# Kernel tuning notes

Measured on AMD Instinct MI355X. Metric: run time of the kernel, lower is better.

The kernel has to match this reference:

```python
import jax, jax.numpy as jnp
import numpy as np

NUM_USERS = 25000
NUM_ITEMS = 25000
N_NODES = NUM_USERS + NUM_ITEMS
N_EDGES = 800000
EMBED_K = 64
N_LAYERS = 3
LRELU_ALPHA = 0.2  # tf.nn.leaky_relu default
EPS = 1e-12        # tf.nn.l2_normalize default epsilon


def setup_inputs() -> dict:
    key = jax.random.key(0)
    ks = jax.random.split(key, 12)
    return {
        "adj_rows": jax.random.randint(ks[0], (N_EDGES,), 0, N_NODES, dtype=jnp.int32),
        "adj_cols": jax.random.randint(ks[1], (N_EDGES,), 0, N_NODES, dtype=jnp.int32),
        "adj_vals": jax.random.uniform(ks[2], (N_EDGES,), dtype=jnp.float32),
        "Gu0": jax.random.normal(ks[3], (NUM_USERS, EMBED_K), dtype=jnp.float32) * 0.1,
        "Gi0": jax.random.normal(ks[4], (NUM_ITEMS, EMBED_K), dtype=jnp.float32) * 0.1,
        "W_gc": jax.random.normal(ks[5], (N_LAYERS, EMBED_K, EMBED_K), dtype=jnp.float32) * 0.1,
        "b_gc": jax.random.normal(ks[6], (N_LAYERS, EMBED_K), dtype=jnp.float32) * 0.1,
        "W_bi": jax.random.normal(ks[7], (N_LAYERS, EMBED_K, EMBED_K), dtype=jnp.float32) * 0.1,
        "b_bi": jax.random.normal(ks[8], (N_LAYERS, EMBED_K), dtype=jnp.float32) * 0.1,
        "user": jax.random.randint(ks[9], (4096,), 0, NUM_USERS, dtype=jnp.int32),
        "item": jax.random.randint(ks[10], (4096,), 0, NUM_ITEMS, dtype=jnp.int32),
    }


def _propagate(adj_rows, adj_cols, adj_vals, Gu0, Gi0, W_gc, b_gc, W_bi, b_bi):
    # ego: [N, d] concatenation of user + item 0th-layer embeddings
    ego = jnp.concatenate([Gu0, Gi0], axis=0)
    all_embeddings = [ego]
    for k in range(W_gc.shape[0]):
        # sparse A_hat @ ego via COO gather + segment_sum (replaces folded sparse_dense_matmul)
        side = jax.ops.segment_sum(adj_vals[:, None] * ego[adj_cols], adj_rows,
                                   num_segments=N_NODES)
        sum_emb = jax.nn.leaky_relu(side @ W_gc[k] + b_gc[k][None, :], LRELU_ALPHA)
        bi_emb = jax.nn.leaky_relu((ego * side) @ W_bi[k] + b_bi[k][None, :], LRELU_ALPHA)
        ego = sum_emb + bi_emb  # message_dropout = 0 -> identity
        norm = ego * jax.lax.rsqrt(
            jnp.maximum(jnp.sum(ego * ego, axis=1, keepdims=True), EPS))
        all_embeddings.append(norm)
        # NOTE: next layer consumes the UN-normalized ego, as in the original
    all_embeddings = jnp.concatenate(all_embeddings, axis=1)  # [N, d*(L+1)]
    gu = all_embeddings[:NUM_USERS]
    gi = all_embeddings[NUM_USERS:]
    return gu, gi


def reference(adj_rows, adj_cols, adj_vals, Gu0, Gi0, W_gc, b_gc, W_bi, b_bi, user, item):
    gu, gi = _propagate(adj_rows, adj_cols, adj_vals, Gu0, Gi0, W_gc, b_gc, W_bi, b_bi)
    # call(): embedding lookup + dot product per (user, item) pair
    gamma_u = gu[user]
    gamma_i = gi[item]
    xui = jnp.sum(gamma_u * gamma_i, axis=1)
    return xui, gu, gi
```

## Files before the change

### kernel.cpp

```cpp
#include <hip/hip_runtime.h>

#define NUM_USERS 25000
#define NUM_ITEMS 25000
#define N_NODES   50000
#define N_EDGES   800000
#define K         64
#define N_QUERY   4096
#define LRELU     0.2f

#define NBUCKET   196
#define A1_CHUNK  8192
#define A2_CHUNK  4096
#define BMAX      4608

typedef unsigned short ushort_t;
typedef unsigned long long u64_t;

__device__ __forceinline__ size_t node_out_offset(int n) {
    return (size_t)N_QUERY + (size_t)n * 256;
}

__device__ __forceinline__ ushort_t f2bf(float x) {
    unsigned u = __float_as_uint(x);
    return (ushort_t)((u + 0x7FFFu + ((u >> 16) & 1u)) >> 16);
}
__device__ __forceinline__ float bf2f(ushort_t v) {
    return __uint_as_float(((unsigned)v) << 16);
}

__global__ __launch_bounds__(256) void init_ego_kernel(
    const float* __restrict__ Gu0, const float* __restrict__ Gi0,
    float* __restrict__ ego, ushort_t* __restrict__ egb, float* __restrict__ out)
{
    int tid = blockIdx.x * 256 + threadIdx.x;
    if (tid >= N_NODES * K) return;
    int n = tid >> 6;
    int d = tid & 63;
    float v = (n < NUM_USERS) ? Gu0[tid] : Gi0[tid - NUM_USERS * K];
    ego[tid] = v;
    egb[tid] = f2bf(v);
    out[node_out_offset(n) + d] = v;
}

__global__ __launch_bounds__(256) void wtrans_kernel(
    const float* __restrict__ W_gc, const float* __restrict__ W_bi,
    float* __restrict__ WT)
{
    int tid = blockIdx.x * 256 + threadIdx.x;
    if (tid >= 3 * 2 * 64 * 64) return;
    int k   = tid >> 13;
    int m   = (tid >> 12) & 1;
    int idx = tid & 4095;
    int o   = idx >> 6;
    int j   = idx & 63;
    const float* src = m ? W_bi : W_gc;
    WT[tid] = src[k * 4096 + j * 64 + o];
}

__global__ __launch_bounds__(256) void bhist_kernel(
    const int* __restrict__ rows, int* __restrict__ bucket_count)
{
    __shared__ int h[NBUCKET];
    int t = threadIdx.x;
    if (t < NBUCKET) h[t] = 0;
    __syncthreads();
    int base = blockIdx.x * A1_CHUNK;
    for (int i = t; i < A1_CHUNK; i += 256) {
        int e = base + i;
        if (e < N_EDGES) atomicAdd(&h[rows[e] >> 8], 1);
    }
    __syncthreads();
    if (t < NBUCKET) atomicAdd(&bucket_count[t], h[t]);
}

__global__ __launch_bounds__(256) void bscan_kernel(
    const int* __restrict__ bucket_count,
    int* __restrict__ gbase, int* __restrict__ cursor)
{
    __shared__ int sh[256];
    int t = threadIdx.x;
    sh[t] = (t < NBUCKET) ? bucket_count[t] : 0;
    __syncthreads();
    for (int off = 1; off < 256; off <<= 1) {
        int v = (t >= off) ? sh[t - off] : 0;
        __syncthreads();
        sh[t] += v;
        __syncthreads();
    }
    int excl = (t == 0) ? 0 : sh[t - 1];
    if (t < NBUCKET) { gbase[t] = excl; cursor[t] = excl; }
    if (t == NBUCKET) gbase[NBUCKET] = N_EDGES;
}

__global__ __launch_bounds__(256) void bscatter_kernel(
    const int* __restrict__ rows, const int* __restrict__ cols,
    const float* __restrict__ vals, int* __restrict__ cursor,
    u64_t* __restrict__ csr64)
{
    __shared__ u64_t recs[A2_CHUNK];
    __shared__ int hist[NBUCKET], lbase[NBUCKET], lcur[NBUCKET];
    int t = threadIdx.x;
    if (t < NBUCKET) { hist[t] = 0; lcur[t] = 0; }
    __syncthreads();
    int base = blockIdx.x * A2_CHUNK;
    for (int i = t; i < A2_CHUNK; i += 256) {
        int e = base + i;
        if (e < N_EDGES) {
            int r = rows[e];
            u64_t rec = ((u64_t)(unsigned)__float_as_uint(vals[e]) << 32)
                      | ((u64_t)(unsigned)cols[e] << 16)
                      | (unsigned)r;
            recs[i] = rec;
            atomicAdd(&hist[r >> 8], 1);
        }
    }
    __syncthreads();
    if (t < NBUCKET) lbase[t] = atomicAdd(&cursor[t], hist[t]);
    __syncthreads();
    for (int i = t; i < A2_CHUNK; i += 256) {
        int e = base + i;
        if (e < N_EDGES) {
            u64_t rec = recs[i];
            int b = (int)((rec >> 8) & 0xFF);
            int dst = lbase[b] + atomicAdd(&lcur[b], 1);
            csr64[dst] = rec;
        }
    }
}

__global__ __launch_bounds__(256) void bsort_kernel(
    const int* __restrict__ gbase, u64_t* __restrict__ csr64,
    int* __restrict__ offs)
{
    __shared__ u64_t recs[BMAX];
    __shared__ int hist[256], lscan[256], lcur[256];
    int b = blockIdx.x, t = threadIdx.x;
    int g0 = gbase[b];
    int nb = gbase[b + 1] - g0;
    if (nb > BMAX) nb = BMAX;
    hist[t] = 0; lcur[t] = 0;
    __syncthreads();
    for (int i = t; i < nb; i += 256) {
        u64_t rec = csr64[g0 + i];
        recs[i] = rec;
        atomicAdd(&hist[(int)(rec & 0xFF)], 1);
    }
    __syncthreads();
    int v0 = hist[t];
    lscan[t] = v0;
    __syncthreads();
    for (int off = 1; off < 256; off <<= 1) {
        int v = (t >= off) ? lscan[t - off] : 0;
        __syncthreads();
        lscan[t] += v;
        __syncthreads();
    }
    int excl = lscan[t] - v0;
    int row = (b << 8) + t;
    if (row < N_NODES) offs[row] = g0 + excl;
    if (b == 0 && t == 0) offs[N_NODES] = N_EDGES;
    __syncthreads();
    lscan[t] = excl;
    __syncthreads();
    for (int i = t; i < nb; i += 256) {
        u64_t rec = recs[i];
        int rl = (int)(rec & 0xFF);
        int pos = lscan[rl] + atomicAdd(&lcur[rl], 1);
        u64_t outrec = (rec >> 32 << 32) | ((rec >> 16) & 0xFFFFu);
        csr64[g0 + pos] = outrec;
    }
}

__global__ __launch_bounds__(512, 8) void gather_kernel(
    const int* __restrict__ offs, const long long* __restrict__ csr_cv,
    const ushort_t* __restrict__ egb, float* __restrict__ side)
{
    int t = threadIdx.x;
    int wave = t >> 6;
    int lane = t & 63;
    int node = blockIdx.x * 8 + wave;

    int beg = offs[node];
    int end = offs[node + 1];
    float acc = 0.f;
    int j = beg;

    for (; j + 12 <= end; j += 12) {
        long long cvp[12];
        #pragma unroll
        for (int u = 0; u < 12; ++u) cvp[u] = __builtin_nontemporal_load(csr_cv + j + u);
        float gg[12];
        #pragma unroll
        for (int u = 0; u < 12; ++u)
            gg[u] = bf2f(egb[((size_t)(unsigned int)(cvp[u] & 0xffffffffLL) << 6) + lane]);
        #pragma unroll
        for (int u = 0; u < 12; ++u)
            acc = fmaf(__uint_as_float((unsigned int)((u64_t)cvp[u] >> 32)), gg[u], acc);
    }
    for (; j + 4 <= end; j += 4) {
        long long cvp[4];
        #pragma unroll
        for (int u = 0; u < 4; ++u) cvp[u] = __builtin_nontemporal_load(csr_cv + j + u);
        float gg[4];
        #pragma unroll
        for (int u = 0; u < 4; ++u)
            gg[u] = bf2f(egb[((size_t)(unsigned int)(cvp[u] & 0xffffffffLL) << 6) + lane]);
        #pragma unroll
        for (int u = 0; u < 4; ++u)
            acc = fmaf(__uint_as_float((unsigned int)((u64_t)cvp[u] >> 32)), gg[u], acc);
    }
    for (; j < end; ++j) {
        long long cvp = __builtin_nontemporal_load(csr_cv + j);
        acc = fmaf(__uint_as_float((unsigned int)((u64_t)cvp >> 32)),
                   bf2f(egb[((size_t)(unsigned int)(cvp & 0xffffffffLL) << 6) + lane]), acc);
    }

    side[((size_t)node << 6) + lane] = acc;
}

__global__ __launch_bounds__(256, 2) void transform_kernel(
    const float* __restrict__ side, float* __restrict__ ego,
    ushort_t* __restrict__ egb,
    const float* __restrict__ WgT, const float* __restrict__ WbT,
    const float* __restrict__ bgc, const float* __restrict__ bbi,
    float* __restrict__ out, int layer_k)
{
    __shared__ float s_s [64 * 64];
    __shared__ float s_es[64 * 64];
    __shared__ float s_wg[64 * 64];
    __shared__ float s_wb[64 * 64];

    int t = threadIdx.x;
    int base = blockIdx.x * 64;

    for (int idx = t; idx < 64 * 16; idx += 256) {
        int r = idx >> 4;
        int q = idx & 15;
        int qs = q ^ ((r >> 2) & 7);
        float4 sv = make_float4(0.f, 0.f, 0.f, 0.f);
        float4 ev = make_float4(0.f, 0.f, 0.f, 0.f);
        int node = base + r;
        if (node < N_NODES) {
            sv = *(const float4*)(side + ((size_t)node << 6) + 4 * q);
            ev = *(const float4*)(ego  + ((size_t)node << 6) + 4 * q);
        }
        *(float4*)&s_s [r * 64 + 4 * qs] = sv;
        *(float4*)&s_es[r * 64 + 4 * qs] =
            make_float4(ev.x * sv.x, ev.y * sv.y, ev.z * sv.z, ev.w * sv.w);
        *(float4*)&s_wg[r * 64 + 4 * qs] = *(const float4*)(WgT + (size_t)r * 64 + 4 * q);
        *(float4*)&s_wb[r * 64 + 4 * qs] = *(const float4*)(WbT + (size_t)r * 64 + 4 * q);
    }
    __syncthreads();

    const int o0  = (t & 15) << 2;
    const int ln0 = (t >> 4) << 2;
    const int sa  = (t >> 4) & 7;
    const int sw  = t & 7;

    float accg[4][4] = {};
    float accb[4][4] = {};

    #pragma unroll 4
    for (int kq = 0; kq < 16; ++kq) {
        const int qa = (kq ^ sa) << 2;
        const int qw = (kq ^ sw) << 2;
        float4 a[4], b[4], wg[4], wb[4];
        #pragma unroll
        for (int i = 0; i < 4; ++i) {
            a[i] = *(const float4*)&s_s [(ln0 + i) * 64 + qa];
            b[i] = *(const float4*)&s_es[(ln0 + i) * 64 + qa];
        }
        #pragma unroll
        for (int j = 0; j < 4; ++j) {
            wg[j] = *(const float4*)&s_wg[(o0 + j) * 64 + qw];
            wb[j] = *(const float4*)&s_wb[(o0 + j) * 64 + qw];
        }
        #pragma unroll
        for (int i = 0; i < 4; ++i) {
            #pragma unroll
            for (int j = 0; j < 4; ++j) {
                accg[i][j] = fmaf(a[i].x, wg[j].x, accg[i][j]);
                accg[i][j] = fmaf(a[i].y, wg[j].y, accg[i][j]);
                accg[i][j] = fmaf(a[i].z, wg[j].z, accg[i][j]);
                accg[i][j] = fmaf(a[i].w, wg[j].w, accg[i][j]);
                accb[i][j] = fmaf(b[i].x, wb[j].x, accb[i][j]);
                accb[i][j] = fmaf(b[i].y, wb[j].y, accb[i][j]);
                accb[i][j] = fmaf(b[i].z, wb[j].z, accb[i][j]);
                accb[i][j] = fmaf(b[i].w, wb[j].w, accb[i][j]);
            }
        }
    }

    float4 bg4 = *(const float4*)(bgc + o0);
    float4 bb4 = *(const float4*)(bbi + o0);
    float bgv[4] = {bg4.x, bg4.y, bg4.z, bg4.w};
    float bbv[4] = {bb4.x, bb4.y, bb4.z, bb4.w};

    #pragma unroll
    for (int i = 0; i < 4; ++i) {
        int node = base + ln0 + i;
        float en[4];
        float ss = 0.f;
        #pragma unroll
        for (int j = 0; j < 4; ++j) {
            float g = accg[i][j] + bgv[j];
            float h = accb[i][j] + bbv[j];
            g = (g > 0.f) ? g : LRELU * g;
            h = (h > 0.f) ? h : LRELU * h;
            en[j] = g + h;
            ss = fmaf(en[j], en[j], ss);
        }
        #pragma unroll
        for (int m = 1; m < 16; m <<= 1) ss += __shfl_xor(ss, m);
        float inv = rsqrtf(fmaxf(ss, 1e-12f));
        if (node < N_NODES) {
            *(float4*)(ego + ((size_t)node << 6) + o0) =
                make_float4(en[0], en[1], en[2], en[3]);
            *(ushort4*)(egb + ((size_t)node << 6) + o0) =
                make_ushort4(f2bf(en[0]), f2bf(en[1]), f2bf(en[2]), f2bf(en[3]));
            *(float4*)(out + node_out_offset(node) + (size_t)(layer_k + 1) * K + o0) =
                make_float4(en[0] * inv, en[1] * inv, en[2] * inv, en[3] * inv);
        }
    }
}

__global__ __launch_bounds__(256) void xui_kernel(
    const int* __restrict__ user, const int* __restrict__ item,
    float* __restrict__ out)
{
    int idx = blockIdx.x * 4 + (threadIdx.x >> 6);
    if (idx >= N_QUERY) return;
    int lane = threadIdx.x & 63;
    int u  = user[idx];
    int it = item[idx];
    const float4* gu = (const float4*)(out + (size_t)N_QUERY + (size_t)u * 256);
    const float4* gi = (const float4*)(out + (size_t)N_QUERY + (size_t)NUM_USERS * 256
                                           + (size_t)it * 256);
    float4 a = gu[lane];
    float4 b = gi[lane];
    float d = a.x * b.x + a.y * b.y + a.z * b.z + a.w * b.w;
    #pragma unroll
    for (int off = 32; off; off >>= 1) d += __shfl_xor(d, off);
    if (lane == 0) out[idx] = d;
}

extern "C" void kernel_launch(void* const* d_in, const int* in_sizes, int n_in,
                              void* d_out, int out_size, void* d_ws, size_t ws_size,
                              hipStream_t stream)
{
    const int*   adj_rows = (const int*)  d_in[0];
    const int*   adj_cols = (const int*)  d_in[1];
    const float* adj_vals = (const float*)d_in[2];
    const float* Gu0      = (const float*)d_in[3];
    const float* Gi0      = (const float*)d_in[4];
    const float* W_gc     = (const float*)d_in[5];
    const float* b_gc     = (const float*)d_in[6];
    const float* W_bi     = (const float*)d_in[7];
    const float* b_bi     = (const float*)d_in[8];
    const int*   user     = (const int*)  d_in[9];
    const int*   item     = (const int*)  d_in[10];

    float* out = (float*)d_out;

    float*    ego    = (float*)d_ws;
    float*    side   = ego + (size_t)N_NODES * K;
    ushort_t* egb    = (ushort_t*)(side + (size_t)N_NODES * K);
    u64_t*    csr64  = (u64_t*)(egb + (size_t)N_NODES * K);
    int*      offs   = (int*)(csr64 + N_EDGES);
    int*      gbase  = offs + N_NODES + 1;
    int*      cursor = gbase + NBUCKET + 1;
    int*      bcnt   = cursor + NBUCKET;
    float*    WT     = (float*)(bcnt + NBUCKET);

    hipMemsetAsync(bcnt, 0, NBUCKET * sizeof(int), stream);
    bhist_kernel<<<(N_EDGES + A1_CHUNK - 1) / A1_CHUNK, 256, 0, stream>>>(adj_rows, bcnt);
    bscan_kernel<<<1, 256, 0, stream>>>(bcnt, gbase, cursor);
    bscatter_kernel<<<(N_EDGES + A2_CHUNK - 1) / A2_CHUNK, 256, 0, stream>>>(
        adj_rows, adj_cols, adj_vals, cursor, csr64);
    bsort_kernel<<<NBUCKET, 256, 0, stream>>>(gbase, csr64, offs);

    wtrans_kernel<<<(3 * 2 * 4096 + 255) / 256, 256, 0, stream>>>(W_gc, W_bi, WT);
    init_ego_kernel<<<(N_NODES * K + 255) / 256, 256, 0, stream>>>(Gu0, Gi0, ego, egb, out);

    for (int k = 0; k < 3; ++k) {
        gather_kernel<<<N_NODES / 8, 512, 0, stream>>>(
            offs, (const long long*)csr64, egb, side);
        transform_kernel<<<(N_NODES + 63) / 64, 256, 0, stream>>>(
            side, ego, egb,
            WT + (size_t)k * 8192, WT + (size_t)k * 8192 + 4096,
            b_gc + (size_t)k * K, b_bi + (size_t)k * K,
            out, k);
    }

    xui_kernel<<<N_QUERY / 4, 256, 0, stream>>>(user, item, out);
}
```

Before: 267.5 us.

## Gather two bf16 dims per lane across half-waves; drop fp32 ego buffer

The gather kernel now splits each wave into two half-waves that process alternating edges. Each lane loads a 32-bit pair of bf16 values, and the two halves are reduced with a cross-half shuffle, which doubles edges in flight per wave and widens each load. The fp32 ego array is removed: transform reads the bf16 copy for the ego*side product and skips writing bf16 on the last layer. The init and weight-transpose kernels are fused into one launch. In exchange, the bilinear term now uses the bf16-rounded ego instead of fp32, which slightly changes precision.

```diff
diff --git a/kernel.cpp b/kernel.cpp
--- a/kernel.cpp
+++ b/kernel.cpp
@@ -28,33 +28,30 @@
     return __uint_as_float(((unsigned)v) << 16);
 }
 
-__global__ __launch_bounds__(256) void init_ego_kernel(
+__global__ __launch_bounds__(256) void init_kernel(
     const float* __restrict__ Gu0, const float* __restrict__ Gi0,
-    float* __restrict__ ego, ushort_t* __restrict__ egb, float* __restrict__ out)
+    const float* __restrict__ W_gc, const float* __restrict__ W_bi,
+    ushort_t* __restrict__ egb, float* __restrict__ WT, float* __restrict__ out)
 {
     int tid = blockIdx.x * 256 + threadIdx.x;
-    if (tid >= N_NODES * K) return;
-    int n = tid >> 6;
-    int d = tid & 63;
-    float v = (n < NUM_USERS) ? Gu0[tid] : Gi0[tid - NUM_USERS * K];
-    ego[tid] = v;
-    egb[tid] = f2bf(v);
-    out[node_out_offset(n) + d] = v;
-}
-
-__global__ __launch_bounds__(256) void wtrans_kernel(
-    const float* __restrict__ W_gc, const float* __restrict__ W_bi,
-    float* __restrict__ WT)
-{
-    int tid = blockIdx.x * 256 + threadIdx.x;
-    if (tid >= 3 * 2 * 64 * 64) return;
-    int k   = tid >> 13;
-    int m   = (tid >> 12) & 1;
-    int idx = tid & 4095;
-    int o   = idx >> 6;
-    int j   = idx & 63;
-    const float* src = m ? W_bi : W_gc;
-    WT[tid] = src[k * 4096 + j * 64 + o];
+    if (tid < N_NODES * K) {
+        int n = tid >> 6;
+        int d = tid & 63;
+        float v = (n < NUM_USERS) ? Gu0[tid] : Gi0[tid - NUM_USERS * K];
+        egb[tid] = f2bf(v);
+        out[node_out_offset(n) + d] = v;
+    } else {
+        int tw = tid - N_NODES * K;
+        if (tw < 3 * 2 * 64 * 64) {
+            int k   = tw >> 13;
+            int m   = (tw >> 12) & 1;
+            int idx = tw & 4095;
+            int o   = idx >> 6;
+            int j   = idx & 63;
+            const float* src = m ? W_bi : W_gc;
+            WT[tw] = src[k * 4096 + j * 64 + o];
+        }
+    }
 }
 
 __global__ __launch_bounds__(256) void bhist_kernel(
@@ -173,54 +170,75 @@
 
 __global__ __launch_bounds__(512, 8) void gather_kernel(
     const int* __restrict__ offs, const long long* __restrict__ csr_cv,
-    const ushort_t* __restrict__ egb, float* __restrict__ side)
+    const unsigned* __restrict__ egb2, float* __restrict__ side)
 {
     int t = threadIdx.x;
     int wave = t >> 6;
     int lane = t & 63;
+    int par  = lane >> 5;
+    int d2   = lane & 31;
     int node = blockIdx.x * 8 + wave;
 
     int beg = offs[node];
     int end = offs[node + 1];
-    float acc = 0.f;
+    float a0 = 0.f, a1 = 0.f;
     int j = beg;
 
-    for (; j + 12 <= end; j += 12) {
-        long long cvp[12];
-        #pragma unroll
-        for (int u = 0; u < 12; ++u) cvp[u] = __builtin_nontemporal_load(csr_cv + j + u);
-        float gg[12];
-        #pragma unroll
-        for (int u = 0; u < 12; ++u)
-            gg[u] = bf2f(egb[((size_t)(unsigned int)(cvp[u] & 0xffffffffLL) << 6) + lane]);
-        #pragma unroll
-        for (int u = 0; u < 12; ++u)
-            acc = fmaf(__uint_as_float((unsigned int)((u64_t)cvp[u] >> 32)), gg[u], acc);
-    }
-    for (; j + 4 <= end; j += 4) {
-        long long cvp[4];
-        #pragma unroll
-        for (int u = 0; u < 4; ++u) cvp[u] = __builtin_nontemporal_load(csr_cv + j + u);
-        float gg[4];
+    for (; j + 16 <= end; j += 16) {
+        long long cv[8];
+        #pragma unroll
+        for (int u = 0; u < 8; ++u)
+            cv[u] = __builtin_nontemporal_load(csr_cv + j + 2 * u + par);
+        unsigned g[8];
+        #pragma unroll
+        for (int u = 0; u < 8; ++u)
+            g[u] = egb2[((size_t)(unsigned)(cv[u] & 0xffffffffLL) << 5) + d2];
+        #pragma unroll
+        for (int u = 0; u < 8; ++u) {
+            float v = __uint_as_float((unsigned)((u64_t)cv[u] >> 32));
+            a0 = fmaf(v, bf2f((ushort_t)(g[u] & 0xFFFFu)), a0);
+            a1 = fmaf(v, bf2f((ushort_t)(g[u] >> 16)), a1);
+        }
+    }
+    for (; j + 8 <= end; j += 8) {
+        long long cv[4];
         #pragma unroll
         for (int u = 0; u < 4; ++u)
-            gg[u] = bf2f(egb[((size_t)(unsigned int)(cvp[u] & 0xffffffffLL) << 6) + lane]);
+            cv[u] = __builtin_nontemporal_load(csr_cv + j + 2 * u + par);
+        unsigned g[4];
         #pragma unroll
         for (int u = 0; u < 4; ++u)
-            acc = fmaf(__uint_as_float((unsigned int)((u64_t)cvp[u] >> 32)), gg[u], acc);
-    }
-    for (; j < end; ++j) {
-        long long cvp = __builtin_nontemporal_load(csr_cv + j);
-        acc = fmaf(__uint_as_float((unsigned int)((u64_t)cvp >> 32)),
-                   bf2f(egb[((size_t)(unsigned int)(cvp & 0xffffffffLL) << 6) + lane]), acc);
-    }
-
-    side[((size_t)node << 6) + lane] = acc;
+            g[u] = egb2[((size_t)(unsigned)(cv[u] & 0xffffffffLL) << 5) + d2];
+        #pragma unroll
+        for (int u = 0; u < 4; ++u) {
+            float v = __uint_as_float((unsigned)((u64_t)cv[u] >> 32));
+            a0 = fmaf(v, bf2f((ushort_t)(g[u] & 0xFFFFu)), a0);
+            a1 = fmaf(v, bf2f((ushort_t)(g[u] >> 16)), a1);
+        }
+    }
+    for (; j + 2 <= end; j += 2) {
+        long long cv = __builtin_nontemporal_load(csr_cv + j + par);
+        unsigned g = egb2[((size_t)(unsigned)(cv & 0xffffffffLL) << 5) + d2];
+        float v = __uint_as_float((unsigned)((u64_t)cv >> 32));
+        a0 = fmaf(v, bf2f((ushort_t)(g & 0xFFFFu)), a0);
+        a1 = fmaf(v, bf2f((ushort_t)(g >> 16)), a1);
+    }
+    if (j < end && par == 0) {
+        long long cv = __builtin_nontemporal_load(csr_cv + j);
+        unsigned g = egb2[((size_t)(unsigned)(cv & 0xffffffffLL) << 5) + d2];
+        float v = __uint_as_float((unsigned)((u64_t)cv >> 32));
+        a0 = fmaf(v, bf2f((ushort_t)(g & 0xFFFFu)), a0);
+        a1 = fmaf(v, bf2f((ushort_t)(g >> 16)), a1);
+    }
+
+    a0 += __shfl_xor(a0, 32);
+    a1 += __shfl_xor(a1, 32);
+    if (par == 0)
+        *(float2*)(side + ((size_t)node << 6) + 2 * d2) = make_float2(a0, a1);
 }
 
 __global__ __launch_bounds__(256, 2) void transform_kernel(
-    const float* __restrict__ side, float* __restrict__ ego,
-    ushort_t* __restrict__ egb,
+    const float* __restrict__ side, ushort_t* __restrict__ egb,
     const float* __restrict__ WgT, const float* __restrict__ WbT,
     const float* __restrict__ bgc, const float* __restrict__ bbi,
     float* __restrict__ out, int layer_k)
@@ -242,7 +260,8 @@
         int node = base + r;
         if (node < N_NODES) {
             sv = *(const float4*)(side + ((size_t)node << 6) + 4 * q);
-            ev = *(const float4*)(ego  + ((size_t)node << 6) + 4 * q);
+            ushort4 uv = *(const ushort4*)(egb + ((size_t)node << 6) + 4 * q);
+            ev = make_float4(bf2f(uv.x), bf2f(uv.y), bf2f(uv.z), bf2f(uv.w));
         }
         *(float4*)&s_s [r * 64 + 4 * qs] = sv;
         *(float4*)&s_es[r * 64 + 4 * qs] =
@@ -314,10 +333,9 @@
         for (int m = 1; m < 16; m <<= 1) ss += __shfl_xor(ss, m);
         float inv = rsqrtf(fmaxf(ss, 1e-12f));
         if (node < N_NODES) {
-            *(float4*)(ego + ((size_t)node << 6) + o0) =
-                make_float4(en[0], en[1], en[2], en[3]);
-            *(ushort4*)(egb + ((size_t)node << 6) + o0) =
-                make_ushort4(f2bf(en[0]), f2bf(en[1]), f2bf(en[2]), f2bf(en[3]));
+            if (layer_k != 2)
+                *(ushort4*)(egb + ((size_t)node << 6) + o0) =
+                    make_ushort4(f2bf(en[0]), f2bf(en[1]), f2bf(en[2]), f2bf(en[3]));
             *(float4*)(out + node_out_offset(node) + (size_t)(layer_k + 1) * K + o0) =
                 make_float4(en[0] * inv, en[1] * inv, en[2] * inv, en[3] * inv);
         }
@@ -362,8 +380,7 @@
 
     float* out = (float*)d_out;
 
-    float*    ego    = (float*)d_ws;
-    float*    side   = ego + (size_t)N_NODES * K;
+    float*    side   = (float*)d_ws;
     ushort_t* egb    = (ushort_t*)(side + (size_t)N_NODES * K);
     u64_t*    csr64  = (u64_t*)(egb + (size_t)N_NODES * K);
     int*      offs   = (int*)(csr64 + N_EDGES);
@@ -379,14 +396,17 @@
         adj_rows, adj_cols, adj_vals, cursor, csr64);
     bsort_kernel<<<NBUCKET, 256, 0, stream>>>(gbase, csr64, offs);
 
-    wtrans_kernel<<<(3 * 2 * 4096 + 255) / 256, 256, 0, stream>>>(W_gc, W_bi, WT);
-    init_ego_kernel<<<(N_NODES * K + 255) / 256, 256, 0, stream>>>(Gu0, Gi0, ego, egb, out);
+    {
+        int total = N_NODES * K + 3 * 2 * 64 * 64;
+        init_kernel<<<(total + 255) / 256, 256, 0, stream>>>(
+            Gu0, Gi0, W_gc, W_bi, egb, WT, out);
+    }
 
     for (int k = 0; k < 3; ++k) {
         gather_kernel<<<N_NODES / 8, 512, 0, stream>>>(
-            offs, (const long long*)csr64, egb, side);
+            offs, (const long long*)csr64, (const unsigned*)egb, side);
         transform_kernel<<<(N_NODES + 63) / 64, 256, 0, stream>>>(
-            side, ego, egb,
+            side, egb,
             WT + (size_t)k * 8192, WT + (size_t)k * 8192 + 4096,
             b_gc + (size_t)k * K, b_bi + (size_t)k * K,
             out, k);
```

New measurement: 252.3 us. 5.7% less time.
